# Optimization experiments

Measured on AMD Instinct MI355X. Metric: run time of the kernel, lower is better.

Reference implementation:

```python
import jax, jax.numpy as jnp
import numpy as np

B, N, D, H, L = 2, 1024, 256, 4, 9
HEAD = D // H  # 64
IMG_H, IMG_W = 480, 640
SINKHORN_ITERS = 20
CH = [3, 32, 64, 128, 256]


def setup_inputs() -> dict:
    key = jax.random.key(0)
    ks = iter(jax.random.split(key, 80))
    def rn(shape, s):
        return jax.random.normal(next(ks), shape, dtype=jnp.float32) * s
    inp = {}
    size = jnp.array([IMG_W, IMG_H], jnp.float32)
    inp['kpts0'] = jax.random.uniform(next(ks), (B, N, 2), dtype=jnp.float32) * size
    inp['kpts1'] = jax.random.uniform(next(ks), (B, N, 2), dtype=jnp.float32) * size
    inp['scores0'] = jax.random.uniform(next(ks), (B, N), dtype=jnp.float32)
    inp['scores1'] = jax.random.uniform(next(ks), (B, N), dtype=jnp.float32)
    inp['desc0'] = rn((B, D, N), 1.0)
    inp['desc1'] = rn((B, D, N), 1.0)
    for i in range(4):
        inp['kenc_w%d' % i] = rn((CH[i + 1], CH[i]), CH[i] ** -0.5)
        inp['kenc_b%d' % i] = rn((CH[i + 1],), 0.02)
        if i < 3:
            inp['kenc_g%d' % i] = jnp.ones((CH[i + 1],), jnp.float32)
            inp['kenc_be%d' % i] = jnp.zeros((CH[i + 1],), jnp.float32)
    s = D ** -0.5
    inp['gnn_proj_w'] = rn((L, 3, D, D), s)
    inp['gnn_proj_b'] = rn((L, 3, D), 0.02)
    inp['gnn_merge_w'] = rn((L, D, D), s)
    inp['gnn_merge_b'] = rn((L, D), 0.02)
    inp['gnn_mlp1_w'] = rn((L, 2 * D, 2 * D), (2 * D) ** -0.5)
    inp['gnn_mlp1_b'] = rn((L, 2 * D), 0.02)
    inp['gnn_ln_g'] = jnp.ones((L, 2 * D), jnp.float32)
    inp['gnn_ln_b'] = jnp.zeros((L, 2 * D), jnp.float32)
    inp['gnn_mlp2_w'] = rn((L, D, 2 * D), (2 * D) ** -0.5)
    inp['gnn_mlp2_b'] = jnp.zeros((L, D), jnp.float32)
    inp['final_w'] = rn((D, D), s)
    inp['final_b'] = rn((D,), 0.02)
    inp['bin_score'] = jnp.array(1.0, jnp.float32)
    return inp


def _conv1(x, w, b):
    # 1x1 Conv1d == per-position matmul: x [B,C,N], w [O,C], b [O]
    return jnp.einsum('oc,bcn->bon', w, x) + b[None, :, None]


def _layernorm(x, g, b, eps=1e-6):
    # matches source LayerNorm: normalize over channel dim (-2), std with ddof=1, eps added to std
    mean = jnp.mean(x, axis=1, keepdims=True)
    std = jnp.std(x, axis=1, keepdims=True, ddof=1)
    return g[None, :, None] * (x - mean) / (std + eps) + b[None, :, None]


def _normalize_kpts(kpts):
    size = jnp.array([IMG_W, IMG_H], jnp.float32)
    center = size / 2.0
    scaling = jnp.max(size) * 0.7
    return (kpts - center) / scaling


def _attn(x, src, pw, pb, mw, mb):
    # pw [3,D,D]; view(B, head_dim, n_heads, N) matches torch .view on [B,D,N]
    q = _conv1(x, pw[0], pb[0]).reshape(B, HEAD, H, -1)
    k = _conv1(src, pw[1], pb[1]).reshape(B, HEAD, H, -1)
    v = _conv1(src, pw[2], pb[2]).reshape(B, HEAD, H, -1)
    scores = jnp.einsum('bdhn,bdhm->bhnm', q, k) / (HEAD ** 0.5)
    prob = jax.nn.softmax(scores, axis=-1)
    msg = jnp.einsum('bhnm,bdhm->bdhn', prob, v).reshape(B, D, -1)
    return _conv1(msg, mw, mb)


def _sinkhorn(Z, log_mu, log_nu, iters):
    def step(uv, _):
        u, v = uv
        u = log_mu - jax.scipy.special.logsumexp(Z + v[:, None, :], axis=2)
        v = log_nu - jax.scipy.special.logsumexp(Z + u[:, :, None], axis=1)
        return (u, v), None
    init = (jnp.zeros_like(log_mu), jnp.zeros_like(log_nu))
    (u, v), _ = jax.lax.scan(step, init, None, length=iters)
    return Z + u[:, :, None] + v[:, None, :]


def _log_ot(scores, alpha, iters):
    b, m, n = scores.shape
    bins0 = jnp.broadcast_to(alpha, (b, m, 1))
    bins1 = jnp.broadcast_to(alpha, (b, 1, n))
    a = jnp.broadcast_to(alpha, (b, 1, 1))
    couplings = jnp.concatenate([jnp.concatenate([scores, bins0], -1),
                                 jnp.concatenate([bins1, a], -1)], 1)
    norm = jnp.asarray(-np.log(float(m + n)), jnp.float32)
    log_mu = jnp.concatenate([jnp.full((m,), norm, jnp.float32),
                              jnp.array([np.log(float(n))], jnp.float32) + norm])
    log_nu = jnp.concatenate([jnp.full((n,), norm, jnp.float32),
                              jnp.array([np.log(float(m))], jnp.float32) + norm])
    log_mu = jnp.broadcast_to(log_mu, (b, m + 1))
    log_nu = jnp.broadcast_to(log_nu, (b, n + 1))
    Z = _sinkhorn(couplings, log_mu, log_nu, iters)
    return Z - norm


def _superglue_fwd(kpts0, kpts1, scores0, scores1, desc0, desc1,
                   kenc_w0, kenc_b0, kenc_g0, kenc_be0,
                   kenc_w1, kenc_b1, kenc_g1, kenc_be1,
                   kenc_w2, kenc_b2, kenc_g2, kenc_be2,
                   kenc_w3, kenc_b3,
                   gnn_proj_w, gnn_proj_b, gnn_merge_w, gnn_merge_b,
                   gnn_mlp1_w, gnn_mlp1_b, gnn_ln_g, gnn_ln_b,
                   gnn_mlp2_w, gnn_mlp2_b, final_w, final_b, bin_score):
    kenc = [(kenc_w0, kenc_b0, kenc_g0, kenc_be0),
            (kenc_w1, kenc_b1, kenc_g1, kenc_be1),
            (kenc_w2, kenc_b2, kenc_g2, kenc_be2),
            (kenc_w3, kenc_b3, None, None)]

    def encode(kpts, sc):
        x = jnp.concatenate([_normalize_kpts(kpts).transpose(0, 2, 1), sc[:, None, :]], 1)  # [B,3,N]
        for (w, b, g, be) in kenc:
            x = _conv1(x, w, b)
            if g is not None:
                x = jax.nn.relu(_layernorm(x, g, be))
        return x

    desc0 = desc0 + encode(kpts0, scores0)
    desc1 = desc1 + encode(kpts1, scores1)

    # only 'cross' GNN layers execute in this fork ('self' layers are skipped via continue)
    for i in range(L):
        def prop(x, src):
            msg = _attn(x, src, gnn_proj_w[i], gnn_proj_b[i], gnn_merge_w[i], gnn_merge_b[i])
            y = jnp.concatenate([x, msg], 1)  # [B,2D,N]
            y = jax.nn.relu(_layernorm(_conv1(y, gnn_mlp1_w[i], gnn_mlp1_b[i]), gnn_ln_g[i], gnn_ln_b[i]))
            return _conv1(y, gnn_mlp2_w[i], gnn_mlp2_b[i])
        d0 = prop(desc0, desc1)
        d1 = prop(desc1, desc0)
        desc0, desc1 = desc0 + d0, desc1 + d1

    mdesc0 = _conv1(desc0, final_w, final_b)
    mdesc1 = _conv1(desc1, final_w, final_b)
    sc = jnp.einsum('bdn,bdm->bnm', mdesc0, mdesc1) / (D ** 0.5)
    return _log_ot(sc, bin_score, SINKHORN_ITERS)  # [B, N+1, N+1] log assignment matrix


def reference(kpts0, kpts1, scores0, scores1, desc0, desc1,
              kenc_w0, kenc_b0, kenc_g0, kenc_be0,
              kenc_w1, kenc_b1, kenc_g1, kenc_be1,
              kenc_w2, kenc_b2, kenc_g2, kenc_be2,
              kenc_w3, kenc_b3,
              gnn_proj_w, gnn_proj_b, gnn_merge_w, gnn_merge_b,
              gnn_mlp1_w, gnn_mlp1_b, gnn_ln_g, gnn_ln_b,
              gnn_mlp2_w, gnn_mlp2_b, final_w, final_b, bin_score):
    return _superglue_fwd(kpts0, kpts1, scores0, scores1, desc0, desc1,
                          kenc_w0, kenc_b0, kenc_g0, kenc_be0,
                          kenc_w1, kenc_b1, kenc_g1, kenc_be1,
                          kenc_w2, kenc_b2, kenc_g2, kenc_be2,
                          kenc_w3, kenc_b3,
                          gnn_proj_w, gnn_proj_b, gnn_merge_w, gnn_merge_b,
                          gnn_mlp1_w, gnn_mlp1_b, gnn_ln_g, gnn_ln_b,
                          gnn_mlp2_w, gnn_mlp2_b, final_w, final_b, bin_score)
```

## Files before the change

kernel.cpp:

```cpp
#include <hip/hip_runtime.h>
#include <hip/hip_bf16.h>
#include <math.h>

#define DEVI static __device__ __forceinline__

namespace {
constexpr int Bc   = 2;
constexpr int Nc   = 1024;
constexpr int Dc   = 256;
constexpr int NP1c = 1025;
constexpr int LDZ  = 1028;
constexpr int LDV  = 1028;
constexpr float LN_EPS = 1e-6f;
constexpr float NORMV  = -7.6246189861593985f;
constexpr float LOGNV  =  6.9314718055994531f;
}

typedef __attribute__((ext_vector_type(8))) short bf16x8;
typedef __attribute__((ext_vector_type(4))) float f32x4;

DEVI void split2(float v, __hip_bfloat16& h, __hip_bfloat16& l) {
    h = __float2bfloat16(v);
    l = __float2bfloat16(v - __bfloat162float(h));
}

#define GLDS16(gp, lp) __builtin_amdgcn_global_load_lds( \
    (const __attribute__((address_space(1))) void*)(gp), \
    (__attribute__((address_space(3))) void*)(lp), 16, 0, 0)

DEVI float block_sum_256(float v, float* scratch) {
    int t = threadIdx.x;
    scratch[t] = v;
    __syncthreads();
    for (int s = 128; s > 0; s >>= 1) {
        if (t < s) scratch[t] += scratch[t + s];
        __syncthreads();
    }
    float r = scratch[0];
    __syncthreads();
    return r;
}

DEVI void ln_relu_inplace(float* x, const float* g, const float* be, int C, float* scratch) {
    int t = threadIdx.x;
    float v = (t < C) ? x[t] : 0.f;
    float mean = block_sum_256(v, scratch) / (float)C;
    float dv = (t < C) ? (x[t] - mean) : 0.f;
    float var = block_sum_256(dv * dv, scratch) / (float)(C - 1);
    float rstd = 1.f / (sqrtf(var) + LN_EPS);
    if (t < C) x[t] = fmaxf(g[t] * dv * rstd + be[t], 0.f);
    __syncthreads();
}

__global__ __launch_bounds__(256) void kenc_kernel(
    const float* __restrict__ kpts, const float* __restrict__ scr,
    const float* __restrict__ desc_in, float* __restrict__ desc_out,
    __hip_bfloat16* __restrict__ catHi, __hip_bfloat16* __restrict__ catLo,
    const float* __restrict__ w0, const float* __restrict__ b0,
    const float* __restrict__ g0, const float* __restrict__ be0,
    const float* __restrict__ w1T, const float* __restrict__ b1,
    const float* __restrict__ g1, const float* __restrict__ be1,
    const float* __restrict__ w2T, const float* __restrict__ b2,
    const float* __restrict__ g2, const float* __restrict__ be2,
    const float* __restrict__ w3T, const float* __restrict__ b3)
{
    __shared__ float xa[256], xb[256], scratch[256];
    const int n = blockIdx.x, b = blockIdx.y, t = threadIdx.x;
    if (t == 0) {
        float kx = kpts[((long)b * Nc + n) * 2 + 0];
        float ky = kpts[((long)b * Nc + n) * 2 + 1];
        xa[0] = (kx - 320.f) * (1.f / 448.f);
        xa[1] = (ky - 240.f) * (1.f / 448.f);
        xa[2] = scr[b * Nc + n];
    }
    __syncthreads();
    if (t < 32) { float a = b0[t]; for (int c = 0; c < 3;  ++c) a += w0[t*3 + c] * xa[c]; xb[t] = a; }
    __syncthreads();
    ln_relu_inplace(xb, g0, be0, 32, scratch);
    if (t < 64) {
        float a = b1[t];
        #pragma unroll 8
        for (int c = 0; c < 32;  ++c) a += w1T[c*64 + t] * xb[c];
        xa[t] = a;
    }
    __syncthreads();
    ln_relu_inplace(xa, g1, be1, 64, scratch);
    if (t < 128) {
        float a = b2[t];
        #pragma unroll 8
        for (int c = 0; c < 64;  ++c) a += w2T[c*128 + t] * xa[c];
        xb[t] = a;
    }
    __syncthreads();
    ln_relu_inplace(xb, g2, be2, 128, scratch);
    {   float a = b3[t];
        #pragma unroll 8
        for (int c = 0; c < 128; ++c) a += w3T[c*256 + t] * xb[c];
        float v = desc_in[((long)b * Dc + t) * Nc + n] + a;
        desc_out[((long)b * Nc + n) * Dc + t] = v;
        __hip_bfloat16 h, l; split2(v, h, l);
        long cr = ((long)b * Nc + n) * 512 + t;
        catHi[cr] = h; catLo[cr] = l;
    }
}

__global__ __launch_bounds__(256) void transposeW(
    const float* __restrict__ src, float* __restrict__ dst, int O, int C)
{
    long i = (long)blockIdx.x * 256 + threadIdx.x;
    if (i >= (long)O * C) return;
    int o = (int)(i / C), c = (int)(i % C);
    dst[(long)c * O + o] = src[i];
}

template<int BM, int BN, int EPI, int BLO>
__global__ __launch_bounds__(256) void mfma_nt(
    const short* __restrict__ Ahi0, const short* __restrict__ Alo0, int lda,
    const short* __restrict__ Bhi0, const short* __restrict__ Blo0, int ldb,
    int K, float scale, const float* __restrict__ bias,
    float* __restrict__ outF, __hip_bfloat16* __restrict__ outHi,
    __hip_bfloat16* __restrict__ outLo,
    __hip_bfloat16* __restrict__ outHi2, __hip_bfloat16* __restrict__ outHi3,
    int ldo,
    long aS1, long bS1, long oS1)
{
    constexpr int MI = BM / 32;
    constexpr int NI = BN / 32;
    constexpr int instA = BM / 16, instB = BN / 16;
    constexpr int OFF_AH = 0;
    constexpr int OFF_AL = BM * 32;
    constexpr int OFF_BH = 2 * BM * 32;
    constexpr int OFF_BL = 2 * BM * 32 + BN * 32;
    constexpr int CHUNK = (2 * BM + (BLO ? 2 : 1) * BN) * 32;
    __shared__ short smem[2 * CHUNK];

    const int z = blockIdx.z;
    const long aOff = z * aS1, bOff = z * bS1, oOff = z * oS1;
    const short* Ah = Ahi0 + aOff; const short* Al = Alo0 + aOff;
    const short* Bh = Bhi0 + bOff; const short* Bl = BLO ? (Blo0 + bOff) : nullptr;

    const int m0 = blockIdx.y * BM, n0 = blockIdx.x * BN;
    const int t = threadIdx.x, lane = t & 63, wid = t >> 6;
    const int lr = lane & 15, lg = lane >> 4;
    const int wr = wid >> 1, wc = wid & 1;

    f32x4 acc[MI][NI];
    for (int mi = 0; mi < MI; ++mi)
        for (int ni = 0; ni < NI; ++ni)
            acc[mi][ni] = f32x4{0.f, 0.f, 0.f, 0.f};

    for (int k0 = 0; k0 < K; k0 += 64) {
        constexpr int total = 2 * instA + (BLO ? 2 : 1) * instB;
        for (int q = wid; q < total; q += 4) {
            const short* gsrc; int ldg, mi, ploff, row0;
            if (q < instA)               { gsrc = Ah; ldg = lda; mi = q;                 ploff = OFF_AH; row0 = m0; }
            else if (q < 2*instA)        { gsrc = Al; ldg = lda; mi = q - instA;         ploff = OFF_AL; row0 = m0; }
            else if (q < 2*instA+instB)  { gsrc = Bh; ldg = ldb; mi = q - 2*instA;       ploff = OFF_BH; row0 = n0; }
            else                         { gsrc = Bl; ldg = ldb; mi = q - 2*instA-instB; ploff = OFF_BL; row0 = n0; }
            const short* g = gsrc + (long)(row0 + mi * 16 + lr) * ldg + (k0 + lg * 8);
            GLDS16(g,      smem + ploff + mi * 512);
            GLDS16(g + 32, smem + CHUNK + ploff + mi * 512);
        }
        __syncthreads();
        #pragma unroll
        for (int kc2 = 0; kc2 < 2; ++kc2) {
            const short* sm2 = smem + kc2 * CHUNK;
            bf16x8 ah[MI], al[MI];
            #pragma unroll
            for (int mi = 0; mi < MI; ++mi) {
                ah[mi] = *(const bf16x8*)(sm2 + OFF_AH + ((wr * MI + mi) * 64 + lane) * 8);
                al[mi] = *(const bf16x8*)(sm2 + OFF_AL + ((wr * MI + mi) * 64 + lane) * 8);
            }
            #pragma unroll
            for (int ni = 0; ni < NI; ++ni) {
                bf16x8 bh = *(const bf16x8*)(sm2 + OFF_BH + ((wc * NI + ni) * 64 + lane) * 8);
                #pragma unroll
                for (int mi = 0; mi < MI; ++mi) {
                    acc[mi][ni] = __builtin_amdgcn_mfma_f32_16x16x32_bf16(ah[mi], bh, acc[mi][ni], 0, 0, 0);
                    acc[mi][ni] = __builtin_amdgcn_mfma_f32_16x16x32_bf16(al[mi], bh, acc[mi][ni], 0, 0, 0);
                }
                if (BLO) {
                    bf16x8 bl = *(const bf16x8*)(sm2 + OFF_BL + ((wc * NI + ni) * 64 + lane) * 8);
                    #pragma unroll
                    for (int mi = 0; mi < MI; ++mi)
                        acc[mi][ni] = __builtin_amdgcn_mfma_f32_16x16x32_bf16(ah[mi], bl, acc[mi][ni], 0, 0, 0);
                }
            }
        }
        __syncthreads();
    }

    for (int mi = 0; mi < MI; ++mi) {
        for (int i = 0; i < 4; ++i) {
            int row = m0 + wr * (BM / 2) + mi * 16 + lg * 4 + i;
            for (int ni = 0; ni < NI; ++ni) {
                int col = n0 + wc * (BN / 2) + ni * 16 + lr;
                float v = acc[mi][ni][i] * scale;
                if (bias) v += bias[col];
                if (EPI == 0) {
                    outF[(long)row * ldo + col + oOff] = v;
                } else if (EPI == 1) {
                    __hip_bfloat16 h, l;
                    split2(v, h, l);
                    outHi[(long)row * ldo + col + oOff] = h;
                    outLo[(long)row * ldo + col + oOff] = l;
                } else if (EPI == 2) {
                    int dirb = row >> 10, rloc = row & 1023;
                    int tq = col >> 8, within = col & 255;
                    int h4 = within >> 6, hd = within & 63;
                    __hip_bfloat16 hh, ll;
                    split2(v, hh, ll);
                    if (tq == 2) {
                        int w2 = rloc >> 8, mloc = rloc & 255;
                        int lane2 = ((mloc & 31) >> 3) * 16 + (hd & 15);
                        long idx = ((((long)(dirb*4+h4)*4 + w2)*8 + (mloc>>5))*4 + (hd>>4))*512 + lane2*8 + (mloc&7);
                        outHi2[idx] = hh;
                    } else {
                        int lane2 = ((hd & 31) >> 3) * 16 + (rloc & 15);
                        long idx = (((long)(dirb*4+h4)*64 + (rloc>>4))*2 + (hd>>5))*512 + lane2*8 + (hd&7);
                        if (tq == 0) { outHi[idx] = hh; outLo[idx] = ll; }
                        else         { outHi3[idx] = hh; }
                    }
                } else {
                    long i256 = (long)row * 256 + col;
                    v += outF[i256];
                    outF[i256] = v;
                    __hip_bfloat16 h, l;
                    split2(v, h, l);
                    outHi[(long)row * 512 + col] = h;
                    outLo[(long)row * 512 + col] = l;
                }
            }
        }
    }
}

__global__ __launch_bounds__(256) void attn_fused(
    const __hip_bfloat16* __restrict__ qFh, const __hip_bfloat16* __restrict__ qFl,
    const __hip_bfloat16* __restrict__ kFh, const __hip_bfloat16* __restrict__ vFh,
    __hip_bfloat16* __restrict__ catHi, __hip_bfloat16* __restrict__ catLo)
{
    __shared__ short pLds[4 * 16 * 256];
    __shared__ float redm[4][16], reds[4][16];
    const int y = blockIdx.y;
    const int dir = y >> 3, b = (y >> 2) & 1, h = y & 3;
    const int q0 = blockIdx.x * 16;
    const int t = threadIdx.x, lane = t & 63, w = t >> 6;
    const int lr = lane & 15, lg = lane >> 4;
    const int dbQ = dir * 2 + b;
    const int srcdb = (1 - dir) * 2 + b;
    const short* qh = (const short*)qFh; const short* ql = (const short*)qFl;
    const short* kh = (const short*)kFh;
    const short* vh = (const short*)vFh;

    const long qbase = (((long)(dbQ * 4 + h)) * 64 + (q0 >> 4)) * 2;
    bf16x8 ah[2], al[2];
    #pragma unroll
    for (int kc = 0; kc < 2; ++kc) {
        ah[kc] = *(const bf16x8*)(qh + (qbase + kc) * 512 + lane * 8);
        al[kc] = *(const bf16x8*)(ql + (qbase + kc) * 512 + lane * 8);
    }

    f32x4 acc[16];
    #pragma unroll
    for (int ni = 0; ni < 16; ++ni) acc[ni] = f32x4{0.f, 0.f, 0.f, 0.f};

    const long kbase0 = (((long)(srcdb * 4 + h)) * 64 + w * 16) * 2;
    #pragma unroll
    for (int ni = 0; ni < 16; ++ni) {
        long kb = (kbase0 + ni * 2) * 512 + lane * 8;
        bf16x8 bh0 = *(const bf16x8*)(kh + kb);
        bf16x8 bh1 = *(const bf16x8*)(kh + kb + 512);
        acc[ni] = __builtin_amdgcn_mfma_f32_16x16x32_bf16(ah[0], bh0, acc[ni], 0, 0, 0);
        acc[ni] = __builtin_amdgcn_mfma_f32_16x16x32_bf16(al[0], bh0, acc[ni], 0, 0, 0);
        acc[ni] = __builtin_amdgcn_mfma_f32_16x16x32_bf16(ah[1], bh1, acc[ni], 0, 0, 0);
        acc[ni] = __builtin_amdgcn_mfma_f32_16x16x32_bf16(al[1], bh1, acc[ni], 0, 0, 0);
    }

    float mx[4] = {-1e30f, -1e30f, -1e30f, -1e30f};
    #pragma unroll
    for (int ni = 0; ni < 16; ++ni)
        #pragma unroll
        for (int i = 0; i < 4; ++i) {
            float v = acc[ni][i] * 0.125f;
            acc[ni][i] = v;
            mx[i] = fmaxf(mx[i], v);
        }
    #pragma unroll
    for (int off = 1; off < 16; off <<= 1)
        #pragma unroll
        for (int i = 0; i < 4; ++i) mx[i] = fmaxf(mx[i], __shfl_xor(mx[i], off));
    if (lr == 0)
        #pragma unroll
        for (int i = 0; i < 4; ++i) redm[w][lg * 4 + i] = mx[i];
    __syncthreads();
    float Mv[4];
    #pragma unroll
    for (int i = 0; i < 4; ++i)
        Mv[i] = fmaxf(fmaxf(redm[0][lg*4+i], redm[1][lg*4+i]),
                      fmaxf(redm[2][lg*4+i], redm[3][lg*4+i]));
    float sm[4] = {0.f, 0.f, 0.f, 0.f};
    #pragma unroll
    for (int ni = 0; ni < 16; ++ni)
        #pragma unroll
        for (int i = 0; i < 4; ++i) {
            float e = __expf(acc[ni][i] - Mv[i]);
            acc[ni][i] = e;
            sm[i] += e;
        }
    #pragma unroll
    for (int off = 1; off < 16; off <<= 1)
        #pragma unroll
        for (int i = 0; i < 4; ++i) sm[i] += __shfl_xor(sm[i], off);
    if (lr == 0)
        #pragma unroll
        for (int i = 0; i < 4; ++i) reds[w][lg * 4 + i] = sm[i];
    __syncthreads();
    float inv[4];
    #pragma unroll
    for (int i = 0; i < 4; ++i)
        inv[i] = 1.f / (reds[0][lg*4+i] + reds[1][lg*4+i] + reds[2][lg*4+i] + reds[3][lg*4+i]);

    char* pB = (char*)pLds + w * 8192;
    #pragma unroll
    for (int ni = 0; ni < 16; ++ni)
        #pragma unroll
        for (int i = 0; i < 4; ++i) {
            int q = lg * 4 + i, m = ni * 16 + lr;
            int byte = (q * 512 + m * 2) ^ ((q & 7) << 4);
            *(short*)(pB + byte) = (short)__bfloat16_as_ushort(__float2bfloat16(acc[ni][i] * inv[i]));
        }
    __syncthreads();

    f32x4 acc2[4];
    #pragma unroll
    for (int bi = 0; bi < 4; ++bi) acc2[bi] = f32x4{0.f, 0.f, 0.f, 0.f};
    const long vbase0 = (((long)(srcdb * 4 + h)) * 4 + w) * 8;
    #pragma unroll
    for (int km = 0; km < 8; ++km) {
        int rb = (lr * 512 + km * 64 + lg * 16) ^ ((lr & 7) << 4);
        bf16x8 pa = *(const bf16x8*)(pB + rb);
        #pragma unroll
        for (int bi = 0; bi < 4; ++bi) {
            long vr = ((vbase0 + km) * 4 + bi) * 512 + lane * 8;
            bf16x8 vhf = *(const bf16x8*)(vh + vr);
            acc2[bi] = __builtin_amdgcn_mfma_f32_16x16x32_bf16(pa, vhf, acc2[bi], 0, 0, 0);
        }
    }
    __syncthreads();
    float* pr = (float*)pLds;
    #pragma unroll
    for (int bi = 0; bi < 4; ++bi)
        #pragma unroll
        for (int i = 0; i < 4; ++i)
            pr[w * 1024 + (lg * 4 + i) * 64 + bi * 16 + lr] = acc2[bi][i];
    __syncthreads();
    #pragma unroll
    for (int k = 0; k < 4; ++k) {
        int e = t + k * 256;
        float v = pr[e] + pr[1024 + e] + pr[2048 + e] + pr[3072 + e];
        int q = e >> 6, d = e & 63;
        long a = ((long)dbQ * 1024 + q0 + q) * 512 + 256 + h * 64 + d;
        __hip_bfloat16 hh, ll; split2(v, hh, ll);
        catHi[a] = hh; catLo[a] = ll;
    }
}

__global__ __launch_bounds__(256) void ln_relu_planes(
    const float* __restrict__ y, const float* __restrict__ g, const float* __restrict__ be,
    __hip_bfloat16* __restrict__ hi, __hip_bfloat16* __restrict__ lo)
{
    __shared__ float s1[256], s2[256];
    const long row = blockIdx.x;
    const int t = threadIdx.x;
    const float* src = y + row * 512;
    float a = src[t], b = src[t + 256];
    s1[t] = a + b; s2[t] = a * a + b * b;
    __syncthreads();
    for (int s = 128; s > 0; s >>= 1) {
        if (t < s) { s1[t] += s1[t + s]; s2[t] += s2[t + s]; }
        __syncthreads();
    }
    float mean = s1[0] / 512.f;
    float var = fmaxf((s2[0] - 512.f * mean * mean) / 511.f, 0.f);
    float rstd = 1.f / (sqrtf(var) + LN_EPS);
    float v1 = fmaxf(g[t] * (a - mean) * rstd + be[t], 0.f);
    float v2 = fmaxf(g[t + 256] * (b - mean) * rstd + be[t + 256], 0.f);
    __hip_bfloat16 h, l;
    split2(v1, h, l); hi[row * 512 + t] = h;       lo[row * 512 + t] = l;
    split2(v2, h, l); hi[row * 512 + t + 256] = h; lo[row * 512 + t + 256] = l;
}

__global__ __launch_bounds__(256) void wconv_plain(
    const float* __restrict__ w, __hip_bfloat16* __restrict__ hi, __hip_bfloat16* __restrict__ lo, long total)
{
    long i = (long)blockIdx.x * 256 + threadIdx.x;
    if (i >= total) return;
    __hip_bfloat16 h, l; split2(w[i], h, l);
    hi[i] = h; lo[i] = l;
}

__global__ __launch_bounds__(256) void wconv_proj(
    const float* __restrict__ w, __hip_bfloat16* __restrict__ hi, __hip_bfloat16* __restrict__ lo)
{
    long i = (long)blockIdx.x * 256 + threadIdx.x;
    if (i >= 9L * 768 * 256) return;
    long l9 = i / (768 * 256);
    int rem = (int)(i % (768 * 256));
    int op = rem / 256, c = rem % 256;
    int tq = op / 256, within = op % 256;
    int h = within / 64, hd = within % 64;
    int o = tq * 256 + hd * 4 + h;
    float v = w[(l9 * 768 + o) * 256 + c];
    __hip_bfloat16 hh, ll; split2(v, hh, ll);
    hi[i] = hh; lo[i] = ll;
}

__global__ void wconv_proj_bias(const float* __restrict__ b, float* __restrict__ bp)
{
    int i = blockIdx.x * 256 + threadIdx.x;
    if (i >= 9 * 768) return;
    int l9 = i / 768, op = i % 768;
    int tq = op / 256, within = op % 256;
    int h = within / 64, hd = within % 64;
    bp[i] = b[(l9 * 3 + tq) * 256 + hd * 4 + h];
}

__global__ __launch_bounds__(256) void wconv_mergeT(
    const float* __restrict__ w, __hip_bfloat16* __restrict__ hi, __hip_bfloat16* __restrict__ lo)
{
    long i = (long)blockIdx.x * 256 + threadIdx.x;
    if (i >= 9L * 256 * 256) return;
    long l9 = i / (256 * 256);
    int rem = (int)(i % (256 * 256));
    int c = rem / 256, j = rem % 256;
    int h = c / 64, hd = c % 64;
    float v = w[(l9 * 256 + j) * 256 + (hd * 4 + h)];
    __hip_bfloat16 hh, ll; split2(v, hh, ll);
    hi[i] = hh; lo[i] = ll;
}

__global__ __launch_bounds__(256) void wconv_m1(
    const float* __restrict__ w,
    __hip_bfloat16* __restrict__ m1cHi, __hip_bfloat16* __restrict__ m1cLo,
    __hip_bfloat16* __restrict__ m1bHi, __hip_bfloat16* __restrict__ m1bLo)
{
    long i = (long)blockIdx.x * 256 + threadIdx.x;
    if (i >= 9L * 512 * 512) return;
    long lo9 = i / 512;
    int c = (int)(i % 512);
    __hip_bfloat16 hh, ll; split2(w[i], hh, ll);
    if (c < 256) { m1cHi[lo9 * 512 + c] = hh; m1cLo[lo9 * 512 + c] = ll; }
    else         { m1bHi[lo9 * 256 + c - 256] = hh; m1bLo[lo9 * 256 + c - 256] = ll; }
}

__global__ __launch_bounds__(64) void bias_fold(
    const float* __restrict__ w1, const float* __restrict__ b1,
    const float* __restrict__ bm, float* __restrict__ out)
{
    int og = blockIdx.x;
    int l = og >> 9, o = og & 511;
    int t = threadIdx.x;
    float s = 0.f;
    for (int j = t; j < 256; j += 64)
        s += w1[((long)l * 512 + o) * 512 + 256 + j] * bm[l * 256 + j];
    for (int off = 32; off > 0; off >>= 1) s += __shfl_down(s, off);
    if (t == 0) out[og] = b1[(long)l * 512 + o] + s;
}

__global__ void bins_fill(float* __restrict__ Z, const float* __restrict__ alpha_p)
{
    float alpha = alpha_p[0];
    int idx = blockIdx.x * 256 + threadIdx.x;
    int b = blockIdx.y;
    float* Zb = Z + (long)b * NP1c * LDZ;
    if (idx < NP1c) Zb[(long)1024 * LDZ + idx] = alpha;
    else { int i = idx - NP1c; if (i < 1024) Zb[(long)i * LDZ + 1024] = alpha; }
}

__global__ void pad_fill(float* __restrict__ Zm, float* __restrict__ ZT)
{
    int i = blockIdx.x * 256 + threadIdx.x;
    if (i >= 2 * NP1c * 3) return;
    int b = i / (NP1c * 3);
    int rem = i % (NP1c * 3);
    int row = rem / 3, c = 1025 + rem % 3;
    long a = (long)b * NP1c * LDZ + (long)row * LDZ + c;
    Zm[a] = -1e30f;
    ZT[a] = -1e30f;
}

__global__ void transpose_np1(const float* __restrict__ Z, float* __restrict__ ZT)
{
    __shared__ float tile[32][33];
    int b = blockIdx.z;
    int i0 = blockIdx.y * 32, j0 = blockIdx.x * 32;
    int tx = threadIdx.x, ty = threadIdx.y;
    const float* Zb = Z + (long)b * NP1c * LDZ;
    float* Tb = ZT + (long)b * NP1c * LDZ;
    for (int ii = ty; ii < 32; ii += 8) {
        int i = i0 + ii, j = j0 + tx;
        if (i < NP1c && j < NP1c) tile[ii][tx] = Zb[(long)i * LDZ + j];
    }
    __syncthreads();
    for (int jj = ty; jj < 32; jj += 8) {
        int j = j0 + jj, i = i0 + tx;
        if (j < NP1c && i < NP1c) Tb[(long)j * LDZ + i] = tile[tx][jj];
    }
}

__global__ void zero_vec(float* __restrict__ v, int n)
{
    int i = blockIdx.x * 256 + threadIdx.x;
    if (i < n) v[i] = 0.f;
}

__global__ __launch_bounds__(256) void sinkhorn_lse(
    const float* __restrict__ M, const float* __restrict__ addv, float* __restrict__ outv)
{
    __shared__ float sm[256], ss[256];
    const int i = blockIdx.x, b = blockIdx.y, t = threadIdx.x;
    const float* row = M + ((long)b * NP1c + i) * LDZ;
    const float* av = addv + (long)b * LDV;
    float4 x = ((const float4*)row)[t];
    float4 a = ((const float4*)av)[t];
    float v0 = x.x + a.x, v1 = x.y + a.y, v2 = x.z + a.z, v3 = x.w + a.w;
    float m = fmaxf(fmaxf(v0, v1), fmaxf(v2, v3));
    float s = __expf(v0 - m) + __expf(v1 - m) + __expf(v2 - m) + __expf(v3 - m);
    if (t == 0) {
        float4 x2 = ((const float4*)row)[256];
        float4 a2 = ((const float4*)av)[256];
        float v4 = x2.x + a2.x;
        if (v4 > m) { s = s * __expf(m - v4) + 1.f; m = v4; }
        else s += __expf(v4 - m);
    }
    sm[t] = m; ss[t] = s;
    __syncthreads();
    for (int st = 128; st > 0; st >>= 1) {
        if (t < st) {
            float m1 = sm[t], s1 = ss[t], m2 = sm[t + st], s2 = ss[t + st];
            float mm = fmaxf(m1, m2);
            sm[t] = mm;
            ss[t] = s1 * __expf(m1 - mm) + s2 * __expf(m2 - mm);
        }
        __syncthreads();
    }
    if (t == 0) {
        float lse = sm[0] + __logf(ss[0]);
        float lmu = (i < 1024) ? NORMV : (LOGNV + NORMV);
        outv[(long)b * LDV + i] = lmu - lse;
    }
}

__global__ __launch_bounds__(256) void final_out_k(
    const float* __restrict__ Z, const float* __restrict__ u,
    const float* __restrict__ v, float* __restrict__ outp)
{
    const int i = blockIdx.x, b = blockIdx.y, t = threadIdx.x;
    const float* row = Z + ((long)b * NP1c + i) * LDZ;
    float* orow = outp + ((long)b * NP1c + i) * NP1c;
    float ui = u[(long)b * LDV + i];
    for (int j = t; j < NP1c; j += 256)
        orow[j] = row[j] + ui + v[(long)b * LDV + j] - NORMV;
}

extern "C" void kernel_launch(void* const* d_in, const int* in_sizes, int n_in,
                              void* d_out, int out_size, void* d_ws, size_t ws_size,
                              hipStream_t stream)
{
    (void)in_sizes; (void)n_in; (void)out_size; (void)ws_size;
    const float* kpts0   = (const float*)d_in[0];
    const float* kpts1   = (const float*)d_in[1];
    const float* scores0 = (const float*)d_in[2];
    const float* scores1 = (const float*)d_in[3];
    const float* desc0   = (const float*)d_in[4];
    const float* desc1   = (const float*)d_in[5];
    const float* kw0 = (const float*)d_in[6];  const float* kb0 = (const float*)d_in[7];
    const float* kg0 = (const float*)d_in[8];  const float* ke0 = (const float*)d_in[9];
    const float* kw1 = (const float*)d_in[10]; const float* kb1 = (const float*)d_in[11];
    const float* kg1 = (const float*)d_in[12]; const float* ke1 = (const float*)d_in[13];
    const float* kw2 = (const float*)d_in[14]; const float* kb2 = (const float*)d_in[15];
    const float* kg2 = (const float*)d_in[16]; const float* ke2 = (const float*)d_in[17];
    const float* kw3 = (const float*)d_in[18]; const float* kb3 = (const float*)d_in[19];
    const float* gnn_proj_w  = (const float*)d_in[20];
    const float* gnn_proj_b  = (const float*)d_in[21];
    const float* gnn_merge_w = (const float*)d_in[22];
    const float* gnn_merge_b = (const float*)d_in[23];
    const float* gnn_mlp1_w  = (const float*)d_in[24];
    const float* gnn_mlp1_b  = (const float*)d_in[25];
    const float* gnn_ln_g    = (const float*)d_in[26];
    const float* gnn_ln_b    = (const float*)d_in[27];
    const float* gnn_mlp2_w  = (const float*)d_in[28];
    const float* gnn_mlp2_b  = (const float*)d_in[29];
    const float* final_w     = (const float*)d_in[30];
    const float* final_b     = (const float*)d_in[31];
    const float* bin_score   = (const float*)d_in[32];

    char* wsb = (char*)d_ws;
    size_t off = 0;
    auto alloc = [&](size_t bytes) -> void* {
        void* p = wsb + off;
        off = (off + bytes + 255) & ~(size_t)255;
        return p;
    };
    typedef __hip_bfloat16 bf;
    const long ROWS = 4L * Nc;
    float* descF  = (float*)alloc(ROWS * 256 * 4);
    float* ybufF  = (float*)alloc(ROWS * 512 * 4);
    float* Zm     = (float*)alloc((long)Bc * NP1c * LDZ * 4);
    float* ZT     = (float*)alloc((long)Bc * NP1c * LDZ * 4);
    float* uvec   = (float*)alloc(Bc * LDV * 4);
    float* vvec   = (float*)alloc(Bc * LDV * 4);
    float* projBp = (float*)alloc(9L * 768 * 4);
    float* b1c    = (float*)alloc(9L * 512 * 4);
    float* kw1T   = (float*)alloc(32L * 64 * 4);
    float* kw2T   = (float*)alloc(64L * 128 * 4);
    float* kw3T   = (float*)alloc(128L * 256 * 4);
    bf* catHi = (bf*)alloc(ROWS * 512 * 2);  bf* catLo = (bf*)alloc(ROWS * 512 * 2);
    bf* qFh = (bf*)alloc(1048576 * 2); bf* qFl = (bf*)alloc(1048576 * 2);
    bf* kFh = (bf*)alloc(1048576 * 2);
    bf* vFh = (bf*)alloc(1048576 * 2);
    bf* ybHi  = (bf*)alloc(ROWS * 512 * 2);  bf* ybLo  = (bf*)alloc(ROWS * 512 * 2);
    bf* mdHi  = (bf*)alloc(ROWS * 256 * 2);  bf* mdLo  = (bf*)alloc(ROWS * 256 * 2);
    bf* projHi = (bf*)alloc(9L*768*256*2);   bf* projLo = (bf*)alloc(9L*768*256*2);
    bf* mrgTHi = (bf*)alloc(9L*256*256*2);   bf* mrgTLo = (bf*)alloc(9L*256*256*2);
    bf* m1bHi  = (bf*)alloc(9L*512*256*2);   bf* m1bLo  = (bf*)alloc(9L*512*256*2);
    bf* m1cHi  = (bf*)alloc(9L*512*512*2);   bf* m1cLo  = (bf*)alloc(9L*512*512*2);
    bf* m2Hi   = (bf*)alloc(9L*256*512*2);   bf* m2Lo   = (bf*)alloc(9L*256*512*2);
    bf* finHi  = (bf*)alloc(256L*256*2);     bf* finLo  = (bf*)alloc(256L*256*2);

    wconv_proj<<<dim3((9*768*256+255)/256), 256, 0, stream>>>(gnn_proj_w, projHi, projLo);
    wconv_proj_bias<<<dim3(27), 256, 0, stream>>>(gnn_proj_b, projBp);
    wconv_mergeT<<<dim3((9*256*256+255)/256), 256, 0, stream>>>(gnn_merge_w, mrgTHi, mrgTLo);
    wconv_m1<<<dim3((int)((9L*512*512+255)/256)), 256, 0, stream>>>(gnn_mlp1_w, m1cHi, m1cLo, m1bHi, m1bLo);
    wconv_plain<<<dim3((9*256*512+255)/256), 256, 0, stream>>>(gnn_mlp2_w, m2Hi, m2Lo, 9L*256*512);
    wconv_plain<<<dim3((256*256+255)/256), 256, 0, stream>>>(final_w, finHi, finLo, 256L*256);
    bias_fold<<<dim3(9*512), 64, 0, stream>>>(gnn_mlp1_w, gnn_mlp1_b, gnn_merge_b, b1c);
    transposeW<<<dim3((64*32+255)/256), 256, 0, stream>>>(kw1, kw1T, 64, 32);
    transposeW<<<dim3((128*64+255)/256), 256, 0, stream>>>(kw2, kw2T, 128, 64);
    transposeW<<<dim3((256*128+255)/256), 256, 0, stream>>>(kw3, kw3T, 256, 128);
    mfma_nt<128,128,1,1><<<dim3(2,4,9), 256, 0, stream>>>(
        (const short*)m1bHi, (const short*)m1bLo, 256,
        (const short*)mrgTHi, (const short*)mrgTLo, 256,
        256, 1.f, nullptr,
        nullptr, m1cHi + 256, m1cLo + 256, nullptr, nullptr, 512,
        512L*256, 256L*256, 512L*512);

    kenc_kernel<<<dim3(Nc, Bc), 256, 0, stream>>>(kpts0, scores0, desc0, descF,
        catHi, catLo,
        kw0, kb0, kg0, ke0, kw1T, kb1, kg1, ke1, kw2T, kb2, kg2, ke2, kw3T, kb3);
    kenc_kernel<<<dim3(Nc, Bc), 256, 0, stream>>>(kpts1, scores1, desc1, descF + 2L*Nc*256,
        catHi + 2L*Nc*512, catLo + 2L*Nc*512,
        kw0, kb0, kg0, ke0, kw1T, kb1, kg1, ke1, kw2T, kb2, kg2, ke2, kw3T, kb3);

    for (int l = 0; l < 9; ++l) {
        mfma_nt<64,64,2,0><<<dim3(12,64,1), 256, 0, stream>>>(
            (const short*)catHi, (const short*)catLo, 512,
            (const short*)(projHi + (long)l*768*256), nullptr, 256,
            256, 1.f, projBp + (long)l*768,
            nullptr, qFh, qFl, vFh, kFh, 0,
            0, 0, 0);
        attn_fused<<<dim3(64, 16), 256, 0, stream>>>(qFh, qFl, kFh, vFh, catHi, catLo);
        mfma_nt<64,64,0,0><<<dim3(8,64,1), 256, 0, stream>>>(
            (const short*)catHi, (const short*)catLo, 512,
            (const short*)(m1cHi + (long)l*512*512), nullptr, 512,
            512, 1.f, b1c + (long)l*512,
            ybufF, nullptr, nullptr, nullptr, nullptr, 512,
            0, 0, 0);
        ln_relu_planes<<<dim3((unsigned)ROWS), 256, 0, stream>>>(
            ybufF, gnn_ln_g + (long)l*512, gnn_ln_b + (long)l*512, ybHi, ybLo);
        mfma_nt<64,64,3,0><<<dim3(4,64,1), 256, 0, stream>>>(
            (const short*)ybHi, (const short*)ybLo, 512,
            (const short*)(m2Hi + (long)l*256*512), nullptr, 512,
            512, 1.f, gnn_mlp2_b + (long)l*256,
            descF, catHi, catLo, nullptr, nullptr, 0,
            0, 0, 0);
    }

    mfma_nt<64,64,1,0><<<dim3(4,64,1), 256, 0, stream>>>(
        (const short*)catHi, (const short*)catLo, 512,
        (const short*)finHi, nullptr, 256,
        256, 1.f, final_b,
        nullptr, mdHi, mdLo, nullptr, nullptr, 256,
        0, 0, 0);
    mfma_nt<64,64,0,1><<<dim3(16,16,2), 256, 0, stream>>>(
        (const short*)mdHi, (const short*)mdLo, 256,
        (const short*)mdHi + 2048L*256, (const short*)mdLo + 2048L*256, 256,
        256, 1.f/16.f, nullptr,
        Zm, nullptr, nullptr, nullptr, nullptr, LDZ,
        1024L*256, 1024L*256, (long)NP1c*LDZ);
    bins_fill<<<dim3(9,2), 256, 0, stream>>>(Zm, bin_score);

    transpose_np1<<<dim3(33,33,2), dim3(32,8), 0, stream>>>(Zm, ZT);
    pad_fill<<<dim3((2*NP1c*3+255)/256), 256, 0, stream>>>(Zm, ZT);
    zero_vec<<<dim3((2*LDV+255)/256), 256, 0, stream>>>(vvec, Bc * LDV);
    zero_vec<<<dim3((2*LDV+255)/256), 256, 0, stream>>>(uvec, Bc * LDV);
    for (int it = 0; it < 20; ++it) {
        sinkhorn_lse<<<dim3(NP1c, Bc), 256, 0, stream>>>(Zm, vvec, uvec);
        sinkhorn_lse<<<dim3(NP1c, Bc), 256, 0, stream>>>(ZT, uvec, vvec);
    }
    final_out_k<<<dim3(NP1c, Bc), 256, 0, stream>>>(Zm, uvec, vvec, (float*)d_out);
}
```

Before: 1.002 ms.

## Drop lo-plane bf16 splits in GNN layers and use wave-level row reductions

Adds an ALO template flag so the per-layer projection, MLP1 and MLP2 GEMMs and the attention QK product skip the low-precision A plane, roughly halving MFMA work and the plane traffic there. It stops writing and allocating the lo planes for Q, the attention output and the LayerNorm output. The LayerNorm and Sinkhorn log-sum-exp kernels now reduce one row per wavefront with shuffles instead of block-wide shared-memory trees, and the pad_fill launch is removed. This trades accuracy for speed, since GNN activations become single bf16, and it relies on the padding columns no longer being read.

```diff
diff --git a/kernel.cpp b/kernel.cpp
--- a/kernel.cpp
+++ b/kernel.cpp
@@ -113,7 +113,7 @@
     dst[(long)c * O + o] = src[i];
 }
 
-template<int BM, int BN, int EPI, int BLO>
+template<int BM, int BN, int EPI, int BLO, int ALO>
 __global__ __launch_bounds__(256) void mfma_nt(
     const short* __restrict__ Ahi0, const short* __restrict__ Alo0, int lda,
     const short* __restrict__ Bhi0, const short* __restrict__ Blo0, int ldb,
@@ -129,15 +129,17 @@
     constexpr int instA = BM / 16, instB = BN / 16;
     constexpr int OFF_AH = 0;
     constexpr int OFF_AL = BM * 32;
-    constexpr int OFF_BH = 2 * BM * 32;
-    constexpr int OFF_BL = 2 * BM * 32 + BN * 32;
-    constexpr int CHUNK = (2 * BM + (BLO ? 2 : 1) * BN) * 32;
+    constexpr int OFF_BH = (1 + ALO) * BM * 32;
+    constexpr int OFF_BL = OFF_BH + BN * 32;
+    constexpr int CHUNK = ((1 + ALO) * BM + (1 + BLO) * BN) * 32;
     __shared__ short smem[2 * CHUNK];
 
     const int z = blockIdx.z;
     const long aOff = z * aS1, bOff = z * bS1, oOff = z * oS1;
-    const short* Ah = Ahi0 + aOff; const short* Al = Alo0 + aOff;
-    const short* Bh = Bhi0 + bOff; const short* Bl = BLO ? (Blo0 + bOff) : nullptr;
+    const short* Ah = Ahi0 + aOff;
+    const short* Al = ALO ? (Alo0 + aOff) : nullptr;
+    const short* Bh = Bhi0 + bOff;
+    const short* Bl = BLO ? (Blo0 + bOff) : nullptr;
 
     const int m0 = blockIdx.y * BM, n0 = blockIdx.x * BN;
     const int t = threadIdx.x, lane = t & 63, wid = t >> 6;
@@ -150,13 +152,17 @@
             acc[mi][ni] = f32x4{0.f, 0.f, 0.f, 0.f};
 
     for (int k0 = 0; k0 < K; k0 += 64) {
-        constexpr int total = 2 * instA + (BLO ? 2 : 1) * instB;
+        constexpr int total = (1 + ALO) * instA + (1 + BLO) * instB;
         for (int q = wid; q < total; q += 4) {
             const short* gsrc; int ldg, mi, ploff, row0;
-            if (q < instA)               { gsrc = Ah; ldg = lda; mi = q;                 ploff = OFF_AH; row0 = m0; }
-            else if (q < 2*instA)        { gsrc = Al; ldg = lda; mi = q - instA;         ploff = OFF_AL; row0 = m0; }
-            else if (q < 2*instA+instB)  { gsrc = Bh; ldg = ldb; mi = q - 2*instA;       ploff = OFF_BH; row0 = n0; }
-            else                         { gsrc = Bl; ldg = ldb; mi = q - 2*instA-instB; ploff = OFF_BL; row0 = n0; }
+            if (q < instA)                      { gsrc = Ah; ldg = lda; mi = q;          ploff = OFF_AH; row0 = m0; }
+            else if (ALO && q < 2 * instA)      { gsrc = Al; ldg = lda; mi = q - instA;  ploff = OFF_AL; row0 = m0; }
+            else {
+                int rb = q - (1 + ALO) * instA;
+                if (rb < instB) { gsrc = Bh; mi = rb;         ploff = OFF_BH; }
+                else            { gsrc = Bl; mi = rb - instB; ploff = OFF_BL; }
+                ldg = ldb; row0 = n0;
+            }
             const short* g = gsrc + (long)(row0 + mi * 16 + lr) * ldg + (k0 + lg * 8);
             GLDS16(g,      smem + ploff + mi * 512);
             GLDS16(g + 32, smem + CHUNK + ploff + mi * 512);
@@ -169,7 +175,7 @@
             #pragma unroll
             for (int mi = 0; mi < MI; ++mi) {
                 ah[mi] = *(const bf16x8*)(sm2 + OFF_AH + ((wr * MI + mi) * 64 + lane) * 8);
-                al[mi] = *(const bf16x8*)(sm2 + OFF_AL + ((wr * MI + mi) * 64 + lane) * 8);
+                if (ALO) al[mi] = *(const bf16x8*)(sm2 + OFF_AL + ((wr * MI + mi) * 64 + lane) * 8);
             }
             #pragma unroll
             for (int ni = 0; ni < NI; ++ni) {
@@ -177,7 +183,7 @@
                 #pragma unroll
                 for (int mi = 0; mi < MI; ++mi) {
                     acc[mi][ni] = __builtin_amdgcn_mfma_f32_16x16x32_bf16(ah[mi], bh, acc[mi][ni], 0, 0, 0);
-                    acc[mi][ni] = __builtin_amdgcn_mfma_f32_16x16x32_bf16(al[mi], bh, acc[mi][ni], 0, 0, 0);
+                    if (ALO) acc[mi][ni] = __builtin_amdgcn_mfma_f32_16x16x32_bf16(al[mi], bh, acc[mi][ni], 0, 0, 0);
                 }
                 if (BLO) {
                     bf16x8 bl = *(const bf16x8*)(sm2 + OFF_BL + ((wc * NI + ni) * 64 + lane) * 8);
@@ -208,8 +214,7 @@
                     int dirb = row >> 10, rloc = row & 1023;
                     int tq = col >> 8, within = col & 255;
                     int h4 = within >> 6, hd = within & 63;
-                    __hip_bfloat16 hh, ll;
-                    split2(v, hh, ll);
+                    __hip_bfloat16 hh = __float2bfloat16(v);
                     if (tq == 2) {
                         int w2 = rloc >> 8, mloc = rloc & 255;
                         int lane2 = ((mloc & 31) >> 3) * 16 + (hd & 15);
@@ -218,8 +223,8 @@
                     } else {
                         int lane2 = ((hd & 31) >> 3) * 16 + (rloc & 15);
                         long idx = (((long)(dirb*4+h4)*64 + (rloc>>4))*2 + (hd>>5))*512 + lane2*8 + (hd&7);
-                        if (tq == 0) { outHi[idx] = hh; outLo[idx] = ll; }
-                        else         { outHi3[idx] = hh; }
+                        if (tq == 0) outHi[idx] = hh;
+                        else         outHi3[idx] = hh;
                     }
                 } else {
                     long i256 = (long)row * 256 + col;
@@ -236,9 +241,9 @@
 }
 
 __global__ __launch_bounds__(256) void attn_fused(
-    const __hip_bfloat16* __restrict__ qFh, const __hip_bfloat16* __restrict__ qFl,
+    const __hip_bfloat16* __restrict__ qFh,
     const __hip_bfloat16* __restrict__ kFh, const __hip_bfloat16* __restrict__ vFh,
-    __hip_bfloat16* __restrict__ catHi, __hip_bfloat16* __restrict__ catLo)
+    __hip_bfloat16* __restrict__ catHi)
 {
     __shared__ short pLds[4 * 16 * 256];
     __shared__ float redm[4][16], reds[4][16];
@@ -249,17 +254,15 @@
     const int lr = lane & 15, lg = lane >> 4;
     const int dbQ = dir * 2 + b;
     const int srcdb = (1 - dir) * 2 + b;
-    const short* qh = (const short*)qFh; const short* ql = (const short*)qFl;
+    const short* qh = (const short*)qFh;
     const short* kh = (const short*)kFh;
     const short* vh = (const short*)vFh;
 
     const long qbase = (((long)(dbQ * 4 + h)) * 64 + (q0 >> 4)) * 2;
-    bf16x8 ah[2], al[2];
-    #pragma unroll
-    for (int kc = 0; kc < 2; ++kc) {
+    bf16x8 ah[2];
+    #pragma unroll
+    for (int kc = 0; kc < 2; ++kc)
         ah[kc] = *(const bf16x8*)(qh + (qbase + kc) * 512 + lane * 8);
-        al[kc] = *(const bf16x8*)(ql + (qbase + kc) * 512 + lane * 8);
-    }
 
     f32x4 acc[16];
     #pragma unroll
@@ -272,9 +275,7 @@
         bf16x8 bh0 = *(const bf16x8*)(kh + kb);
         bf16x8 bh1 = *(const bf16x8*)(kh + kb + 512);
         acc[ni] = __builtin_amdgcn_mfma_f32_16x16x32_bf16(ah[0], bh0, acc[ni], 0, 0, 0);
-        acc[ni] = __builtin_amdgcn_mfma_f32_16x16x32_bf16(al[0], bh0, acc[ni], 0, 0, 0);
         acc[ni] = __builtin_amdgcn_mfma_f32_16x16x32_bf16(ah[1], bh1, acc[ni], 0, 0, 0);
-        acc[ni] = __builtin_amdgcn_mfma_f32_16x16x32_bf16(al[1], bh1, acc[ni], 0, 0, 0);
     }
 
     float mx[4] = {-1e30f, -1e30f, -1e30f, -1e30f};
@@ -361,34 +362,42 @@
         float v = pr[e] + pr[1024 + e] + pr[2048 + e] + pr[3072 + e];
         int q = e >> 6, d = e & 63;
         long a = ((long)dbQ * 1024 + q0 + q) * 512 + 256 + h * 64 + d;
-        __hip_bfloat16 hh, ll; split2(v, hh, ll);
-        catHi[a] = hh; catLo[a] = ll;
-    }
-}
-
-__global__ __launch_bounds__(256) void ln_relu_planes(
+        catHi[a] = __float2bfloat16(v);
+    }
+}
+
+__global__ __launch_bounds__(256) void ln_relu_w(
     const float* __restrict__ y, const float* __restrict__ g, const float* __restrict__ be,
-    __hip_bfloat16* __restrict__ hi, __hip_bfloat16* __restrict__ lo)
-{
-    __shared__ float s1[256], s2[256];
-    const long row = blockIdx.x;
-    const int t = threadIdx.x;
+    __hip_bfloat16* __restrict__ hi)
+{
+    const int t = threadIdx.x, lane = t & 63, w = t >> 6;
+    const long row = (long)blockIdx.x * 4 + w;
     const float* src = y + row * 512;
-    float a = src[t], b = src[t + 256];
-    s1[t] = a + b; s2[t] = a * a + b * b;
-    __syncthreads();
-    for (int s = 128; s > 0; s >>= 1) {
-        if (t < s) { s1[t] += s1[t + s]; s2[t] += s2[t + s]; }
-        __syncthreads();
-    }
-    float mean = s1[0] / 512.f;
-    float var = fmaxf((s2[0] - 512.f * mean * mean) / 511.f, 0.f);
+    float4 v0 = ((const float4*)src)[lane * 2];
+    float4 v1 = ((const float4*)src)[lane * 2 + 1];
+    float s = v0.x + v0.y + v0.z + v0.w + v1.x + v1.y + v1.z + v1.w;
+    float q = v0.x*v0.x + v0.y*v0.y + v0.z*v0.z + v0.w*v0.w
+            + v1.x*v1.x + v1.y*v1.y + v1.z*v1.z + v1.w*v1.w;
+    #pragma unroll
+    for (int off = 1; off < 64; off <<= 1) {
+        s += __shfl_xor(s, off);
+        q += __shfl_xor(q, off);
+    }
+    float mean = s / 512.f;
+    float var = fmaxf((q - 512.f * mean * mean) / 511.f, 0.f);
     float rstd = 1.f / (sqrtf(var) + LN_EPS);
-    float v1 = fmaxf(g[t] * (a - mean) * rstd + be[t], 0.f);
-    float v2 = fmaxf(g[t + 256] * (b - mean) * rstd + be[t + 256], 0.f);
-    __hip_bfloat16 h, l;
-    split2(v1, h, l); hi[row * 512 + t] = h;       lo[row * 512 + t] = l;
-    split2(v2, h, l); hi[row * 512 + t + 256] = h; lo[row * 512 + t + 256] = l;
+    float4 g0 = ((const float4*)g)[lane * 2], g1 = ((const float4*)g)[lane * 2 + 1];
+    float4 b0 = ((const float4*)be)[lane * 2], b1 = ((const float4*)be)[lane * 2 + 1];
+    float xv[8] = {v0.x, v0.y, v0.z, v0.w, v1.x, v1.y, v1.z, v1.w};
+    float gv[8] = {g0.x, g0.y, g0.z, g0.w, g1.x, g1.y, g1.z, g1.w};
+    float bv[8] = {b0.x, b0.y, b0.z, b0.w, b1.x, b1.y, b1.z, b1.w};
+    bf16x8 outv;
+    #pragma unroll
+    for (int k = 0; k < 8; ++k) {
+        float o = fmaxf(gv[k] * (xv[k] - mean) * rstd + bv[k], 0.f);
+        outv[k] = (short)__bfloat16_as_ushort(__float2bfloat16(o));
+    }
+    *(bf16x8*)((short*)hi + row * 512 + lane * 8) = outv;
 }
 
 __global__ __launch_bounds__(256) void wconv_plain(
@@ -478,18 +487,6 @@
     else { int i = idx - NP1c; if (i < 1024) Zb[(long)i * LDZ + 1024] = alpha; }
 }
 
-__global__ void pad_fill(float* __restrict__ Zm, float* __restrict__ ZT)
-{
-    int i = blockIdx.x * 256 + threadIdx.x;
-    if (i >= 2 * NP1c * 3) return;
-    int b = i / (NP1c * 3);
-    int rem = i % (NP1c * 3);
-    int row = rem / 3, c = 1025 + rem % 3;
-    long a = (long)b * NP1c * LDZ + (long)row * LDZ + c;
-    Zm[a] = -1e30f;
-    ZT[a] = -1e30f;
-}
-
 __global__ void transpose_np1(const float* __restrict__ Z, float* __restrict__ ZT)
 {
     __shared__ float tile[32][33];
@@ -518,35 +515,39 @@
 __global__ __launch_bounds__(256) void sinkhorn_lse(
     const float* __restrict__ M, const float* __restrict__ addv, float* __restrict__ outv)
 {
-    __shared__ float sm[256], ss[256];
-    const int i = blockIdx.x, b = blockIdx.y, t = threadIdx.x;
+    const int t = threadIdx.x, lane = t & 63, w = t >> 6;
+    long rowid = (long)blockIdx.x * 4 + w;
+    if (rowid >= 2 * NP1c) return;
+    int b = rowid >= NP1c ? 1 : 0;
+    int i = (int)(rowid - (long)b * NP1c);
     const float* row = M + ((long)b * NP1c + i) * LDZ;
     const float* av = addv + (long)b * LDV;
-    float4 x = ((const float4*)row)[t];
-    float4 a = ((const float4*)av)[t];
-    float v0 = x.x + a.x, v1 = x.y + a.y, v2 = x.z + a.z, v3 = x.w + a.w;
-    float m = fmaxf(fmaxf(v0, v1), fmaxf(v2, v3));
-    float s = __expf(v0 - m) + __expf(v1 - m) + __expf(v2 - m) + __expf(v3 - m);
-    if (t == 0) {
-        float4 x2 = ((const float4*)row)[256];
-        float4 a2 = ((const float4*)av)[256];
-        float v4 = x2.x + a2.x;
+    float m = -1e30f, s = 0.f;
+    #pragma unroll
+    for (int k = 0; k < 4; ++k) {
+        float4 x = ((const float4*)row)[lane * 4 + k];
+        float4 a = ((const float4*)av)[lane * 4 + k];
+        float u0 = x.x + a.x, u1 = x.y + a.y, u2 = x.z + a.z, u3 = x.w + a.w;
+        float mk = fmaxf(fmaxf(u0, u1), fmaxf(u2, u3));
+        float sk = __expf(u0 - mk) + __expf(u1 - mk) + __expf(u2 - mk) + __expf(u3 - mk);
+        if (mk > m) { s = s * __expf(m - mk) + sk; m = mk; }
+        else        { s += sk * __expf(mk - m); }
+    }
+    if (lane == 0) {
+        float v4 = row[1024] + av[1024];
         if (v4 > m) { s = s * __expf(m - v4) + 1.f; m = v4; }
-        else s += __expf(v4 - m);
-    }
-    sm[t] = m; ss[t] = s;
-    __syncthreads();
-    for (int st = 128; st > 0; st >>= 1) {
-        if (t < st) {
-            float m1 = sm[t], s1 = ss[t], m2 = sm[t + st], s2 = ss[t + st];
-            float mm = fmaxf(m1, m2);
-            sm[t] = mm;
-            ss[t] = s1 * __expf(m1 - mm) + s2 * __expf(m2 - mm);
-        }
-        __syncthreads();
-    }
-    if (t == 0) {
-        float lse = sm[0] + __logf(ss[0]);
+        else        { s += __expf(v4 - m); }
+    }
+    #pragma unroll
+    for (int off = 1; off < 64; off <<= 1) {
+        float m2 = __shfl_xor(m, off);
+        float s2 = __shfl_xor(s, off);
+        float mm = fmaxf(m, m2);
+        s = s * __expf(m - mm) + s2 * __expf(m2 - mm);
+        m = mm;
+    }
+    if (lane == 0) {
+        float lse = m + __logf(s);
         float lmu = (i < 1024) ? NORMV : (LOGNV + NORMV);
         outv[(long)b * LDV + i] = lmu - lse;
     }
@@ -617,10 +618,10 @@
     float* kw2T   = (float*)alloc(64L * 128 * 4);
     float* kw3T   = (float*)alloc(128L * 256 * 4);
     bf* catHi = (bf*)alloc(ROWS * 512 * 2);  bf* catLo = (bf*)alloc(ROWS * 512 * 2);
-    bf* qFh = (bf*)alloc(1048576 * 2); bf* qFl = (bf*)alloc(1048576 * 2);
+    bf* qFh = (bf*)alloc(1048576 * 2);
     bf* kFh = (bf*)alloc(1048576 * 2);
     bf* vFh = (bf*)alloc(1048576 * 2);
-    bf* ybHi  = (bf*)alloc(ROWS * 512 * 2);  bf* ybLo  = (bf*)alloc(ROWS * 512 * 2);
+    bf* ybHi  = (bf*)alloc(ROWS * 512 * 2);
     bf* mdHi  = (bf*)alloc(ROWS * 256 * 2);  bf* mdLo  = (bf*)alloc(ROWS * 256 * 2);
     bf* projHi = (bf*)alloc(9L*768*256*2);   bf* projLo = (bf*)alloc(9L*768*256*2);
     bf* mrgTHi = (bf*)alloc(9L*256*256*2);   bf* mrgTLo = (bf*)alloc(9L*256*256*2);
@@ -639,7 +640,7 @@
     transposeW<<<dim3((64*32+255)/256), 256, 0, stream>>>(kw1, kw1T, 64, 32);
     transposeW<<<dim3((128*64+255)/256), 256, 0, stream>>>(kw2, kw2T, 128, 64);
     transposeW<<<dim3((256*128+255)/256), 256, 0, stream>>>(kw3, kw3T, 256, 128);
-    mfma_nt<128,128,1,1><<<dim3(2,4,9), 256, 0, stream>>>(
+    mfma_nt<128,128,1,1,1><<<dim3(2,4,9), 256, 0, stream>>>(
         (const short*)m1bHi, (const short*)m1bLo, 256,
         (const short*)mrgTHi, (const short*)mrgTLo, 256,
         256, 1.f, nullptr,
@@ -654,36 +655,36 @@
         kw0, kb0, kg0, ke0, kw1T, kb1, kg1, ke1, kw2T, kb2, kg2, ke2, kw3T, kb3);
 
     for (int l = 0; l < 9; ++l) {
-        mfma_nt<64,64,2,0><<<dim3(12,64,1), 256, 0, stream>>>(
-            (const short*)catHi, (const short*)catLo, 512,
+        mfma_nt<64,64,2,0,0><<<dim3(12,64,1), 256, 0, stream>>>(
+            (const short*)catHi, nullptr, 512,
             (const short*)(projHi + (long)l*768*256), nullptr, 256,
             256, 1.f, projBp + (long)l*768,
-            nullptr, qFh, qFl, vFh, kFh, 0,
+            nullptr, qFh, nullptr, vFh, kFh, 0,
             0, 0, 0);
-        attn_fused<<<dim3(64, 16), 256, 0, stream>>>(qFh, qFl, kFh, vFh, catHi, catLo);
-        mfma_nt<64,64,0,0><<<dim3(8,64,1), 256, 0, stream>>>(
-            (const short*)catHi, (const short*)catLo, 512,
+        attn_fused<<<dim3(64, 16), 256, 0, stream>>>(qFh, kFh, vFh, catHi);
+        mfma_nt<64,64,0,0,0><<<dim3(8,64,1), 256, 0, stream>>>(
+            (const short*)catHi, nullptr, 512,
             (const short*)(m1cHi + (long)l*512*512), nullptr, 512,
             512, 1.f, b1c + (long)l*512,
             ybufF, nullptr, nullptr, nullptr, nullptr, 512,
             0, 0, 0);
-        ln_relu_planes<<<dim3((unsigned)ROWS), 256, 0, stream>>>(
-            ybufF, gnn_ln_g + (long)l*512, gnn_ln_b + (long)l*512, ybHi, ybLo);
-        mfma_nt<64,64,3,0><<<dim3(4,64,1), 256, 0, stream>>>(
-            (const short*)ybHi, (const short*)ybLo, 512,
+        ln_relu_w<<<dim3(1024), 256, 0, stream>>>(
+            ybufF, gnn_ln_g + (long)l*512, gnn_ln_b + (long)l*512, ybHi);
+        mfma_nt<64,64,3,0,0><<<dim3(4,64,1), 256, 0, stream>>>(
+            (const short*)ybHi, nullptr, 512,
             (const short*)(m2Hi + (long)l*256*512), nullptr, 512,
             512, 1.f, gnn_mlp2_b + (long)l*256,
             descF, catHi, catLo, nullptr, nullptr, 0,
             0, 0, 0);
     }
 
-    mfma_nt<64,64,1,0><<<dim3(4,64,1), 256, 0, stream>>>(
+    mfma_nt<64,64,1,0,1><<<dim3(4,64,1), 256, 0, stream>>>(
         (const short*)catHi, (const short*)catLo, 512,
         (const short*)finHi, nullptr, 256,
         256, 1.f, final_b,
         nullptr, mdHi, mdLo, nullptr, nullptr, 256,
         0, 0, 0);
-    mfma_nt<64,64,0,1><<<dim3(16,16,2), 256, 0, stream>>>(
+    mfma_nt<64,64,0,1,1><<<dim3(16,16,2), 256, 0, stream>>>(
         (const short*)mdHi, (const short*)mdLo, 256,
         (const short*)mdHi + 2048L*256, (const short*)mdLo + 2048L*256, 256,
         256, 1.f/16.f, nullptr,
@@ -692,12 +693,11 @@
     bins_fill<<<dim3(9,2), 256, 0, stream>>>(Zm, bin_score);
 
     transpose_np1<<<dim3(33,33,2), dim3(32,8), 0, stream>>>(Zm, ZT);
-    pad_fill<<<dim3((2*NP1c*3+255)/256), 256, 0, stream>>>(Zm, ZT);
     zero_vec<<<dim3((2*LDV+255)/256), 256, 0, stream>>>(vvec, Bc * LDV);
     zero_vec<<<dim3((2*LDV+255)/256), 256, 0, stream>>>(uvec, Bc * LDV);
     for (int it = 0; it < 20; ++it) {
-        sinkhorn_lse<<<dim3(NP1c, Bc), 256, 0, stream>>>(Zm, vvec, uvec);
-        sinkhorn_lse<<<dim3(NP1c, Bc), 256, 0, stream>>>(ZT, uvec, vvec);
+        sinkhorn_lse<<<dim3(513), 256, 0, stream>>>(Zm, vvec, uvec);
+        sinkhorn_lse<<<dim3(513), 256, 0, stream>>>(ZT, uvec, vvec);
     }
     final_out_k<<<dim3(NP1c, Bc), 256, 0, stream>>>(Zm, uvec, vvec, (float*)d_out);
 }
```

Result: faster. 907.4 us (-9.4%).
